# Optimization experiments

Hardware: AMD Instinct MI355X
Metric: run time of the kernel (lower is better)

The kernel has to match this reference:

```python
import jax, jax.numpy as jnp
import numpy as np

K0 = 0.7978845608028654  # sqrt(2/pi)
C1 = 0.044715

def _gelu_tanh(x):
    # tanh-approx GELU, matching the Triton kernel's math
    return 0.5 * x * (1.0 + jnp.tanh(K0 * (x + C1 * x * x * x)))

def setup_inputs() -> dict:
    key = jax.random.key(0)
    k1, k2, k3 = jax.random.split(key, 3)
    B, C_in, H, W = 32, 64, 128, 128
    C_out, KH = 128, 3
    x = jax.random.normal(k1, (B, C_in, H, W), dtype=jnp.float32)
    weight = jax.random.normal(k2, (C_out, C_in, KH, KH), dtype=jnp.float32)
    bias = jax.random.normal(k3, (C_out,), dtype=jnp.float32)
    return {"x": x, "weight": weight, "bias": bias}

def reference(x, weight, bias):
    # Valid conv2d, stride 1 (NCHW, OIHW)
    y = jax.lax.conv_general_dilated(
        x, weight,
        window_strides=(1, 1), padding="VALID",
        dimension_numbers=("NCHW", "OIHW", "NCHW"))
    y = y + bias[None, :, None, None]
    y = _gelu_tanh(y)
    # global average pool over spatial dims -> [B, C_out]
    return jnp.mean(y, axis=(2, 3))
```

## Files before the change

kernel.cpp:

```cpp
#include <hip/hip_runtime.h>
#include <cstdint>
#include <cstddef>

#define GK0 0.7978845608028654f
#define GC1 0.044715f

typedef __attribute__((ext_vector_type(8))) short short8;
typedef __attribute__((ext_vector_type(4))) float floatx4;

__device__ __forceinline__ unsigned short f2bf(float f) {
  union { float f; unsigned int u; } v; v.f = f;
  unsigned int r = v.u + 0x7fffu + ((v.u >> 16) & 1u);
  return (unsigned short)(r >> 16);
}

__device__ __forceinline__ void gl_lds16(const unsigned short* g, unsigned short* l) {
  __builtin_amdgcn_global_load_lds(
      (const __attribute__((address_space(1))) unsigned int*)g,
      (__attribute__((address_space(3))) unsigned int*)l, 16, 0, 0);
}

__global__ void k_wt(const float* __restrict__ w, unsigned short* __restrict__ wt,
                     float* __restrict__ out) {
  if (blockIdx.x == 0) {
    for (int i = threadIdx.x; i < 32 * 128; i += 256) out[i] = 0.0f;
  }
  int t = blockIdx.x * 256 + threadIdx.x;
  if (t >= 128 * 64 * 9) return;
  int co = t / 576; int r = t - co * 576; int ci = r / 9; int khw = r - ci * 9;
  wt[(khw * 128 + co) * 64 + ci] = f2bf(w[t]);
}

__global__ __launch_bounds__(256, 2) void k_conv(
    const float* __restrict__ x, const unsigned short* __restrict__ wt,
    const float* __restrict__ bias, float* __restrict__ out) {
  __shared__ __align__(16) unsigned short Bs[4 * 72 * 64];
  __shared__ __align__(16) unsigned short As[2][8192];
  const int tid = threadIdx.x, lane = tid & 63, wv = tid >> 6;
  const int w0 = blockIdx.x * 64, h0 = blockIdx.y * 2, b = blockIdx.z;
  const int wm = wv & 1, wn = wv >> 1;
  const int m = lane & 15, q = lane >> 4;

  floatx4 acc[4][4];
#pragma unroll
  for (int i = 0; i < 4; i++)
#pragma unroll
    for (int j = 0; j < 4; j++) acc[i][j] = (floatx4){0.f, 0.f, 0.f, 0.f};

  for (int r = 0; r < 4; r++) {
    const float* xrow = x + ((size_t)(b * 64) * 128 + (h0 + r)) * 128;
    unsigned short* brow = Bs + r * 4608;
    for (int c = tid; c < 1152; c += 256) {
      const int ci = c / 18, i = c - ci * 18;
      const int wc = min(w0 + 4 * i, 124);
      union { float4 v; float f[4]; } u;
      u.v = *(const float4*)(xrow + (size_t)ci * 16384 + wc);
#pragma unroll
      for (int k2 = 0; k2 < 4; k2++) {
        const int p = 4 * i + k2;
        brow[p * 64 + (ci ^ ((p & 7) << 3))] = f2bf(u.f[k2]);
      }
    }
  }

  auto stageA = [&](unsigned short* dst, int khw) {
    const unsigned short* src = wt + khw * 8192;
#pragma unroll
    for (int i = 0; i < 4; i++) {
      const int chunk = wv * 4 + i;
      gl_lds16(src + chunk * 512 + (lane >> 3) * 64 + (((lane & 7) ^ (lane >> 3)) << 3),
               dst + chunk * 512);
    }
  };

  stageA(As[0], 0);
  __syncthreads();

#pragma unroll
  for (int kh = 0; kh < 3; kh++)
#pragma unroll
    for (int kw = 0; kw < 3; kw++) {
      const int khw = kh * 3 + kw;
      if (khw < 8) stageA(As[(khw + 1) & 1], khw + 1);
      const unsigned short* acur = As[khw & 1] + wm * 4096;
      const unsigned short* bcur = Bs + (wn + kh) * 4608;
#pragma unroll
      for (int half = 0; half < 2; half++) {
        const int colb = half * 32 + q * 8;
        short8 a[4], bf[4];
#pragma unroll
        for (int mt = 0; mt < 4; mt++)
          a[mt] = *(const short8*)(acur + (mt * 16 + m) * 64 + (colb ^ ((m & 7) << 3)));
#pragma unroll
        for (int nt = 0; nt < 4; nt++)
          bf[nt] = *(const short8*)(bcur + (nt * 16 + m + kw) * 64 +
                                    (colb ^ (((m + kw) & 7) << 3)));
#pragma unroll
        for (int mt = 0; mt < 4; mt++)
#pragma unroll
          for (int nt = 0; nt < 4; nt++)
            acc[mt][nt] = __builtin_amdgcn_mfma_f32_16x16x32_bf16(
                a[mt], bf[nt], acc[mt][nt], 0, 0, 0);
      }
      __syncthreads();
    }

  const float inv_area = 1.0f / (126.0f * 126.0f);
  float* orow = out + b * 128;
#pragma unroll
  for (int mt = 0; mt < 4; mt++)
#pragma unroll
    for (int r2 = 0; r2 < 4; r2++) {
      const int co = wm * 64 + mt * 16 + q * 4 + r2;
      const float bv = bias[co];
      float s = 0.f;
#pragma unroll
      for (int nt = 0; nt < 4; nt++) {
        float y = acc[mt][nt][r2] + bv;
        float u = GK0 * (y + GC1 * y * y * y);
        float e = __expf(-2.0f * u);
        float g = y * __builtin_amdgcn_rcpf(1.0f + e);
        if (w0 + nt * 16 + m < 126) s += g;
      }
#pragma unroll
      for (int d = 1; d < 16; d <<= 1) s += __shfl_xor(s, d, 64);
      if (m == 0) atomicAdd(&orow[co], s * inv_area);
    }
}

extern "C" void kernel_launch(void* const* d_in, const int* in_sizes, int n_in,
                              void* d_out, int out_size, void* d_ws, size_t ws_size,
                              hipStream_t stream) {
  const float* x    = (const float*)d_in[0];
  const float* w    = (const float*)d_in[1];
  const float* bias = (const float*)d_in[2];
  float* out = (float*)d_out;

  unsigned short* wbuf = (unsigned short*)d_ws;
  if (ws_size < (size_t)9 * 128 * 64 * 2 + 4096) return;

  k_wt<<<288, 256, 0, stream>>>(w, wbuf, out);
  k_conv<<<dim3(2, 63, 32), 256, 0, stream>>>(x, wbuf, bias, out);
}
```

Before: 400.7 us.

## Give each wave a private weight LDS slice and drop per-step block barriers

Each wave now loads its own copy of the weight tile (half of the output channels) into a per-wave LDS buffer. This replaces the block-wide double buffer and removes the __syncthreads after every kernel tap, using explicit lgkmcnt/vmcnt waits instead. The input tile staging is restructured to issue six float4 loads before converting and storing, which gives more loads in flight. The cost is duplicate global weight traffic, since both waves sharing wm load the same data. The next stage's load is also only overlapped with the MFMAs of the current step, not double buffered.

```diff
diff --git a/kernel.cpp b/kernel.cpp
--- a/kernel.cpp
+++ b/kernel.cpp
@@ -35,11 +35,19 @@
     const float* __restrict__ x, const unsigned short* __restrict__ wt,
     const float* __restrict__ bias, float* __restrict__ out) {
   __shared__ __align__(16) unsigned short Bs[4 * 72 * 64];
-  __shared__ __align__(16) unsigned short As[2][8192];
+  __shared__ __align__(16) unsigned short As[4][4096];
   const int tid = threadIdx.x, lane = tid & 63, wv = tid >> 6;
   const int w0 = blockIdx.x * 64, h0 = blockIdx.y * 2, b = blockIdx.z;
   const int wm = wv & 1, wn = wv >> 1;
   const int m = lane & 15, q = lane >> 4;
+  unsigned short* Asw = As[wv];
+
+  const int srcswz = (lane >> 3) * 64 + (((lane & 7) ^ (lane >> 3)) << 3);
+  auto stageA = [&](int khw) {
+    const unsigned short* src = wt + khw * 8192 + wm * 4096 + srcswz;
+#pragma unroll
+    for (int c = 0; c < 8; c++) gl_lds16(src + c * 512, Asw + c * 512);
+  };
 
   floatx4 acc[4][4];
 #pragma unroll
@@ -47,62 +55,66 @@
 #pragma unroll
     for (int j = 0; j < 4; j++) acc[i][j] = (floatx4){0.f, 0.f, 0.f, 0.f};
 
-  for (int r = 0; r < 4; r++) {
-    const float* xrow = x + ((size_t)(b * 64) * 128 + (h0 + r)) * 128;
-    unsigned short* brow = Bs + r * 4608;
-    for (int c = tid; c < 1152; c += 256) {
-      const int ci = c / 18, i = c - ci * 18;
+  stageA(0);
+
+  const float* xb0 = x + (size_t)b * 64 * 16384 + (size_t)h0 * 128;
+#pragma unroll
+  for (int t3 = 0; t3 < 3; t3++) {
+    float4 u[6];
+#pragma unroll
+    for (int j = 0; j < 6; j++) {
+      const int v = (t3 * 6 + j) * 256 + tid;
+      const int r = v / 1152, rem = v - r * 1152;
+      const int ci = rem / 18, i = rem - ci * 18;
       const int wc = min(w0 + 4 * i, 124);
-      union { float4 v; float f[4]; } u;
-      u.v = *(const float4*)(xrow + (size_t)ci * 16384 + wc);
+      u[j] = *(const float4*)(xb0 + (size_t)ci * 16384 + r * 128 + wc);
+    }
+#pragma unroll
+    for (int j = 0; j < 6; j++) {
+      const int v = (t3 * 6 + j) * 256 + tid;
+      const int r = v / 1152, rem = v - r * 1152;
+      const int ci = rem / 18, i = rem - ci * 18;
+      unsigned short* brow = Bs + r * 4608;
+      union { float4 v4; float f[4]; } w4; w4.v4 = u[j];
 #pragma unroll
       for (int k2 = 0; k2 < 4; k2++) {
         const int p = 4 * i + k2;
-        brow[p * 64 + (ci ^ ((p & 7) << 3))] = f2bf(u.f[k2]);
+        brow[p * 64 + (ci ^ ((p & 7) << 3))] = f2bf(w4.f[k2]);
       }
     }
   }
-
-  auto stageA = [&](unsigned short* dst, int khw) {
-    const unsigned short* src = wt + khw * 8192;
-#pragma unroll
-    for (int i = 0; i < 4; i++) {
-      const int chunk = wv * 4 + i;
-      gl_lds16(src + chunk * 512 + (lane >> 3) * 64 + (((lane & 7) ^ (lane >> 3)) << 3),
-               dst + chunk * 512);
-    }
-  };
-
-  stageA(As[0], 0);
   __syncthreads();
-
 #pragma unroll
   for (int kh = 0; kh < 3; kh++)
 #pragma unroll
     for (int kw = 0; kw < 3; kw++) {
       const int khw = kh * 3 + kw;
-      if (khw < 8) stageA(As[(khw + 1) & 1], khw + 1);
-      const unsigned short* acur = As[khw & 1] + wm * 4096;
       const unsigned short* bcur = Bs + (wn + kh) * 4608;
+      short8 a[2][4], bf[2][4];
 #pragma unroll
       for (int half = 0; half < 2; half++) {
         const int colb = half * 32 + q * 8;
-        short8 a[4], bf[4];
 #pragma unroll
         for (int mt = 0; mt < 4; mt++)
-          a[mt] = *(const short8*)(acur + (mt * 16 + m) * 64 + (colb ^ ((m & 7) << 3)));
+          a[half][mt] =
+              *(const short8*)(Asw + (mt * 16 + m) * 64 + (colb ^ ((m & 7) << 3)));
 #pragma unroll
         for (int nt = 0; nt < 4; nt++)
-          bf[nt] = *(const short8*)(bcur + (nt * 16 + m + kw) * 64 +
-                                    (colb ^ (((m + kw) & 7) << 3)));
+          bf[half][nt] = *(const short8*)(bcur + (nt * 16 + m + kw) * 64 +
+                                          (colb ^ (((m + kw) & 7) << 3)));
+      }
+      asm volatile("s_waitcnt lgkmcnt(0)" ::: "memory");
+      if (khw < 8) stageA(khw + 1);
+#pragma unroll
+      for (int half = 0; half < 2; half++)
 #pragma unroll
         for (int mt = 0; mt < 4; mt++)
 #pragma unroll
           for (int nt = 0; nt < 4; nt++)
             acc[mt][nt] = __builtin_amdgcn_mfma_f32_16x16x32_bf16(
-                a[mt], bf[nt], acc[mt][nt], 0, 0, 0);
-      }
-      __syncthreads();
+                a[half][mt], bf[half][nt], acc[mt][nt], 0, 0, 0);
+      if (khw < 8)
+        asm volatile("s_waitcnt vmcnt(0)" ::: "memory");
     }
 
   const float inv_area = 1.0f / (126.0f * 126.0f);
```

New measurement: 369.4 us. 7.8% less time.
